# Kernel optimization log

Hardware: AMD Instinct MI355X
Metric: run time of the kernel (lower is better)

## Reference

```python
import jax, jax.numpy as jnp
import numpy as np

# Orbital structure for basis {A: [2s, 2p, 1d]} -> full_basis l values
LS = [0, 0, 1, 1, 2]
DIMS = [2 * l + 1 for l in LS]            # [1,1,3,3,5]
OFFS = np.concatenate([[0], np.cumsum(DIMS)]).astype(int)
NORB = int(sum(DIMS))                      # 13

# Upper-triangular orbital-pair layout of the flat feature vector
PAIRS = []
_off = 0
for _i in range(len(LS)):
    for _j in range(_i, len(LS)):
        PAIRS.append((_i, _j, _off))
        _off += DIMS[_i] * DIMS[_j]
FEAT_DIM = _off                            # 107

N_ATOMS, N_EDGES, N_KPTS = 256, 4096, 4


def _assemble_blocks(feat):
    """[B, FEAT_DIM] -> [B, NORB, NORB], upper-tri orbital blocks, 0.5 on diagonal pairs."""
    B = feat.shape[0]
    blk = jnp.zeros((B, NORB, NORB), feat.dtype)
    for (i, j, o) in PAIRS:
        di, dj = DIMS[i], DIMS[j]
        f = 0.5 if i == j else 1.0
        blk = blk.at[:, OFFS[i]:OFFS[i] + di, OFFS[j]:OFFS[j] + dj].set(
            f * feat[:, o:o + di * dj].reshape(B, di, dj))
    return blk


def setup_inputs() -> dict:
    key = jax.random.key(0)
    k1, k2, k3, k4, k5 = jax.random.split(key, 5)
    return {
        "orbpair_hopping": jax.random.normal(k1, (N_EDGES, FEAT_DIM), jnp.float32),
        "orbpair_onsite": jax.random.normal(k2, (N_ATOMS, FEAT_DIM), jnp.float32),
        "kpoints": jax.random.uniform(k3, (N_KPTS, 3), jnp.float32),
        "edge_cell_shift": jax.random.randint(k4, (N_EDGES, 3), -3, 4).astype(jnp.float32),
        "edge_index": jax.random.randint(k5, (2, N_EDGES), 0, N_ATOMS),
    }


def reference(orbpair_hopping, orbpair_onsite, kpoints, edge_cell_shift, edge_index):
    hop = _assemble_blocks(orbpair_hopping)      # [E, norb, norb]
    onsite = _assemble_blocks(orbpair_onsite)    # [N, norb, norb]
    N, K = onsite.shape[0], kpoints.shape[0]
    cplx = jnp.complex64

    # phase[k, e] = exp(-i 2pi k . R_e)
    phase = jnp.exp(-2j * jnp.pi * (kpoints @ edge_cell_shift.T)).astype(cplx)  # [K, E]

    # H(k) in block form [K, N, N, norb, norb]
    blk = jnp.zeros((K, N, N, NORB, NORB), cplx)
    ar = jnp.arange(N)
    blk = blk.at[:, ar, ar].set(onsite.astype(cplx)[None])  # diagonal onsite blocks
    ei, ej = edge_index[0], edge_index[1]
    blk = blk.at[:, ei, ej].add(phase[:, :, None, None] * hop.astype(cplx)[None])

    H = blk.transpose(0, 1, 3, 2, 4).reshape(K, N * NORB, N * NORB)
    return H + jnp.conj(jnp.swapaxes(H, 1, 2))  # hermitianize
```

## Files before the change

kernel.cpp:

```cpp
#include <hip/hip_runtime.h>

#define NORB 13
#define FEAT 107
#define TWO_PI 6.28318530717958647692f
#define NN 3328
#define NN2 (NN * NN)

__device__ __forceinline__ void map_pq(int p, int q, int& idx, float& scl) {
    const int DIMS[5] = {1, 1, 3, 3, 5};
    const int OFFS[5] = {0, 1, 2, 5, 8};
    idx = -1; scl = 0.0f;
    int o = 0;
    #pragma unroll
    for (int i = 0; i < 5; ++i) {
        #pragma unroll
        for (int j = i; j < 5; ++j) {
            int di = DIMS[i], dj = DIMS[j];
            if (p >= OFFS[i] && p < OFFS[i] + di && q >= OFFS[j] && q < OFFS[j] + dj) {
                idx = o + (p - OFFS[i]) * dj + (q - OFFS[j]);
                scl = (i == j) ? 0.5f : 1.0f;
            }
            o += di * dj;
        }
    }
}


__global__ void init_kernel(int4* __restrict__ head4, int* __restrict__ pairlist,
                            int* __restrict__ counter) {
    int t = blockIdx.x * blockDim.x + threadIdx.x;
    head4[t] = make_int4(-1, -1, -1, -1);
    if (t < 256) pairlist[t] = t * 257;
    if (t == 0) *counter = 256;
}

__global__ void fill_kernel(const int* __restrict__ eidx, const float* __restrict__ kpt,
                            const float* __restrict__ shf,
                            int* __restrict__ head, int* __restrict__ nxt,
                            int* __restrict__ pairlist, int* __restrict__ counter,
                            float* __restrict__ phases, int E, int K) {
    int tid = blockIdx.x * blockDim.x + threadIdx.x;
    if (tid >= 2 * E) return;
    int e = tid >> 1, dir = tid & 1;
    int ei = eidx[e], ej = eidx[E + e];
    int a = dir ? ej : ei;
    int b = dir ? ei : ej;
    int pid = a * 256 + b;
    int old = atomicExch(&head[pid], tid);
    nxt[tid] = old;
    if (old < 0 && a != b) {
        int pos = atomicAdd(counter, 1);
        pairlist[pos] = pid;
    }
    if (dir == 0) {
        float rx = shf[e * 3 + 0], ry = shf[e * 3 + 1], rz = shf[e * 3 + 2];
        for (int k = 0; k < K; ++k) {
            float th = -TWO_PI * (kpt[k * 3] * rx + kpt[k * 3 + 1] * ry + kpt[k * 3 + 2] * rz);
            float s, c;
            __sincosf(th, &s, &c);
            phases[(e * K + k) * 2]     = c;
            phases[(e * K + k) * 2 + 1] = s;
        }
    }
}

__global__ void zero_gated_kernel(float4* __restrict__ out4, const int* __restrict__ head,
                                  long n4) {
    long i = (long)blockIdx.x * blockDim.x + threadIdx.x;
    long stride = (long)gridDim.x * blockDim.x;
    float4 z = make_float4(0.f, 0.f, 0.f, 0.f);
    for (; i < n4; i += stride) {
        unsigned ci  = (unsigned)(i * 2);
        unsigned rem = ci % NN2;
        unsigned row = rem / NN;
        unsigned c   = rem - row * NN;
        unsigned a   = row / 13u;
        unsigned b0  = c / 13u;
        unsigned b1  = (c + 1u) / 13u;
        bool p0 = (a == b0) || head[a * 256u + b0] >= 0;
        bool p1 = (b1 == b0) ? p0 : ((a == b1) || head[a * 256u + b1] >= 0);
        if (!(p0 && p1)) out4[i] = z;
    }
}

__global__ void paint_kernel(const float* __restrict__ hop, const float* __restrict__ ons,
                             const int* __restrict__ head, const int* __restrict__ nxt,
                             const int* __restrict__ pairlist, const int* __restrict__ counter,
                             const float* __restrict__ phases, float* __restrict__ out,
                             int K) {
    int w = blockIdx.x;
    if (w >= *counter) return;
    int t = threadIdx.x;
    if (t >= NORB * NORB) return;
    int pid = pairlist[w];
    int a = pid >> 8, b = pid & 255;
    int p = t / NORB, q = t - p * NORB;
    int i0, i1; float s0, s1;
    map_pq(p, q, i0, s0);
    map_pq(q, p, i1, s1);
    float ar[4] = {0.f, 0.f, 0.f, 0.f}, ai[4] = {0.f, 0.f, 0.f, 0.f};
    if (a == b) {
        const float* f = ons + (long)a * FEAT;
        float v = 0.f;
        if (i0 >= 0) v += s0 * f[i0];
        if (i1 >= 0) v += s1 * f[i1];
        #pragma unroll
        for (int k = 0; k < 4; ++k) ar[k] += v;
    }
    for (int it = head[pid]; it >= 0; it = nxt[it]) {
        int e = it >> 1, dir = it & 1;
        float hv;
        if (dir == 0) hv = (i0 >= 0) ? s0 * hop[(long)e * FEAT + i0] : 0.f;
        else          hv = (i1 >= 0) ? s1 * hop[(long)e * FEAT + i1] : 0.f;
        const float* ph = phases + (long)e * K * 2;
        if (dir == 0) {
            #pragma unroll
            for (int k = 0; k < 4; ++k) { ar[k] += ph[2 * k] * hv; ai[k] += ph[2 * k + 1] * hv; }
        } else {
            #pragma unroll
            for (int k = 0; k < 4; ++k) { ar[k] += ph[2 * k] * hv; ai[k] -= ph[2 * k + 1] * hv; }
        }
    }
    long row = (long)a * NORB + p;
    long col = (long)b * NORB + q;
    #pragma unroll
    for (int k = 0; k < 4; ++k) {
        long off = (((long)k * NN + row) * NN + col) * 2;
        out[off]     = ar[k];
        out[off + 1] = ai[k];
    }
}


__global__ void zero_kernel(float4* __restrict__ out, long n4) {
    long i = (long)blockIdx.x * blockDim.x + threadIdx.x;
    long stride = (long)gridDim.x * blockDim.x;
    float4 z = make_float4(0.f, 0.f, 0.f, 0.f);
    for (; i < n4; i += stride) out[i] = z;
}

template <int CPX>
__global__ void onsite_kernel(const float* __restrict__ onsite, float* __restrict__ out,
                              int K, long nn) {
    int a = blockIdx.x;
    int t = threadIdx.x;
    if (t >= NORB * NORB) return;
    int p = t / NORB, q = t % NORB;
    int i1, i2; float s1, s2;
    map_pq(p, q, i1, s1);
    map_pq(q, p, i2, s2);
    const float* f = onsite + (long)a * FEAT;
    float v = 0.0f;
    if (i1 >= 0) v += s1 * f[i1];
    if (i2 >= 0) v += s2 * f[i2];
    long row = (long)a * NORB + p;
    long col = (long)a * NORB + q;
    for (int k = 0; k < K; ++k) {
        long off = (((long)k * nn + row) * nn + col) * CPX;
        out[off] = v;
    }
}

template <int CPX>
__global__ void edge_kernel(const float* __restrict__ hop, const float* __restrict__ kpts,
                            const float* __restrict__ shift, const int* __restrict__ eidx,
                            float* __restrict__ out, int E, int K, long nn) {
    int e = blockIdx.x;
    int t = threadIdx.x;
    __shared__ float phc[16], phs[16];
    int ei = eidx[e];
    int ej = eidx[E + e];
    if (t < K && t < 16) {
        float rx = shift[(long)e * 3 + 0];
        float ry = shift[(long)e * 3 + 1];
        float rz = shift[(long)e * 3 + 2];
        float th = -TWO_PI * (kpts[t * 3 + 0] * rx + kpts[t * 3 + 1] * ry + kpts[t * 3 + 2] * rz);
        float s, c;
        __sincosf(th, &s, &c);
        phc[t] = c; phs[t] = s;
    }
    __syncthreads();
    if (t >= NORB * NORB) return;
    int p = t / NORB, q = t % NORB;
    int idx; float scl;
    map_pq(p, q, idx, scl);
    if (idx < 0) return;
    float v = scl * hop[(long)e * FEAT + idx];
    long r1 = (long)ei * NORB + p, c1 = (long)ej * NORB + q;
    long r2 = (long)ej * NORB + q, c2 = (long)ei * NORB + p;
    for (int k = 0; k < K; ++k) {
        float pr = phc[k], pi = phs[k];
        long o1 = (((long)k * nn + r1) * nn + c1) * CPX;
        long o2 = (((long)k * nn + r2) * nn + c2) * CPX;
        atomicAdd(&out[o1], pr * v);
        atomicAdd(&out[o2], pr * v);
        if (CPX == 2) {
            atomicAdd(&out[o1 + 1], pi * v);
            atomicAdd(&out[o2 + 1], -pi * v);
        }
    }
}


extern "C" void kernel_launch(void* const* d_in, const int* in_sizes, int n_in,
                              void* d_out, int out_size, void* d_ws, size_t ws_size,
                              hipStream_t stream) {
    const float* hop  = (const float*)d_in[0];
    const float* ons  = (const float*)d_in[1];
    const float* kpt  = (const float*)d_in[2];
    const float* shf  = (const float*)d_in[3];
    const int*   eidx = (const int*)d_in[4];

    int E = in_sizes[0] / FEAT;
    int N = in_sizes[1] / FEAT;
    int K = in_sizes[2] / 3;
    long nn = (long)N * NORB;

    float* out = (float*)d_out;
    long knn2 = (long)K * nn * nn * 2;

    size_t off_head  = 0;
    size_t off_next  = off_head + 65536 * sizeof(int);
    size_t off_plist = off_next + (size_t)2 * E * sizeof(int);
    size_t off_cnt   = off_plist + (size_t)(256 + 2 * E) * sizeof(int);
    size_t off_phase = (off_cnt + 4 + 127) & ~(size_t)127;
    size_t ws_need   = off_phase + (size_t)E * K * 2 * sizeof(float);

    bool fast = (N == 256) && (K == 4) && (nn == NN) &&
                ((long)out_size == knn2) && (ws_size >= ws_need);

    if (fast) {
        char* ws = (char*)d_ws;
        int*   head   = (int*)(ws + off_head);
        int*   nxt    = (int*)(ws + off_next);
        int*   plist  = (int*)(ws + off_plist);
        int*   cnt    = (int*)(ws + off_cnt);
        float* phases = (float*)(ws + off_phase);

        init_kernel<<<64, 256, 0, stream>>>((int4*)head, plist, cnt);
        int fill_blocks = (2 * E + 255) / 256;
        fill_kernel<<<fill_blocks, 256, 0, stream>>>(eidx, kpt, shf, head, nxt,
                                                     plist, cnt, phases, E, K);
        long n4 = (long)out_size / 4;
        zero_gated_kernel<<<2048, 256, 0, stream>>>((float4*)out, head, n4);
        paint_kernel<<<256 + 2 * E, 192, 0, stream>>>(hop, ons, head, nxt, plist,
                                                      cnt, phases, out, K);
    } else {
        int cpx = ((long)out_size >= knn2) ? 2 : 1;
        long n4 = (long)out_size / 4;
        zero_kernel<<<2048, 256, 0, stream>>>((float4*)out, n4);
        if (cpx == 2) {
            onsite_kernel<2><<<N, 192, 0, stream>>>(ons, out, K, nn);
            edge_kernel<2><<<E, 192, 0, stream>>>(hop, kpt, shf, eidx, out, E, K, nn);
        } else {
            onsite_kernel<1><<<N, 192, 0, stream>>>(ons, out, K, nn);
            edge_kernel<1><<<E, 192, 0, stream>>>(hop, kpt, shf, eidx, out, E, K, nn);
        }
    }
}
```

Baseline: 80.97 us.

## Fuse gated zeroing and block painting into one kernel with per-row zero blocks

```diff
diff --git a/kernel.cpp b/kernel.cpp
--- a/kernel.cpp
+++ b/kernel.cpp
@@ -4,7 +4,7 @@
 #define FEAT 107
 #define TWO_PI 6.28318530717958647692f
 #define NN 3328
-#define NN2 (NN * NN)
+#define NROW 13312
 
 __device__ __forceinline__ void map_pq(int p, int q, int& idx, float& scl) {
     const int DIMS[5] = {1, 1, 3, 3, 5};
@@ -64,70 +64,75 @@
     }
 }
 
-__global__ void zero_gated_kernel(float4* __restrict__ out4, const int* __restrict__ head,
-                                  long n4) {
-    long i = (long)blockIdx.x * blockDim.x + threadIdx.x;
-    long stride = (long)gridDim.x * blockDim.x;
-    float4 z = make_float4(0.f, 0.f, 0.f, 0.f);
-    for (; i < n4; i += stride) {
-        unsigned ci  = (unsigned)(i * 2);
-        unsigned rem = ci % NN2;
-        unsigned row = rem / NN;
-        unsigned c   = rem - row * NN;
-        unsigned a   = row / 13u;
-        unsigned b0  = c / 13u;
-        unsigned b1  = (c + 1u) / 13u;
-        bool p0 = (a == b0) || head[a * 256u + b0] >= 0;
-        bool p1 = (b1 == b0) ? p0 : ((a == b1) || head[a * 256u + b1] >= 0);
-        if (!(p0 && p1)) out4[i] = z;
-    }
-}
-
-__global__ void paint_kernel(const float* __restrict__ hop, const float* __restrict__ ons,
-                             const int* __restrict__ head, const int* __restrict__ nxt,
-                             const int* __restrict__ pairlist, const int* __restrict__ counter,
-                             const float* __restrict__ phases, float* __restrict__ out,
-                             int K) {
-    int w = blockIdx.x;
-    if (w >= *counter) return;
+__global__ __launch_bounds__(256)
+void fused_kernel(const float* __restrict__ hop, const float* __restrict__ ons,
+                  const int* __restrict__ head, const int* __restrict__ nxt,
+                  const int* __restrict__ pairlist, const int* __restrict__ counter,
+                  const float* __restrict__ phases, float* __restrict__ out,
+                  int npaint) {
     int t = threadIdx.x;
-    if (t >= NORB * NORB) return;
-    int pid = pairlist[w];
-    int a = pid >> 8, b = pid & 255;
-    int p = t / NORB, q = t - p * NORB;
-    int i0, i1; float s0, s1;
-    map_pq(p, q, i0, s0);
-    map_pq(q, p, i1, s1);
-    float ar[4] = {0.f, 0.f, 0.f, 0.f}, ai[4] = {0.f, 0.f, 0.f, 0.f};
-    if (a == b) {
-        const float* f = ons + (long)a * FEAT;
-        float v = 0.f;
-        if (i0 >= 0) v += s0 * f[i0];
-        if (i1 >= 0) v += s1 * f[i1];
+    if ((int)blockIdx.x < npaint) {
+        int w = blockIdx.x;
+        if (w >= *counter) return;
+        if (t >= NORB * NORB) return;
+        int pid = pairlist[w];
+        int a = pid >> 8, b = pid & 255;
+        int p = t / NORB, q = t - p * NORB;
+        int i0, i1; float s0, s1;
+        map_pq(p, q, i0, s0);
+        map_pq(q, p, i1, s1);
+        float ar[4] = {0.f, 0.f, 0.f, 0.f}, ai[4] = {0.f, 0.f, 0.f, 0.f};
+        if (a == b) {
+            const float* f = ons + (long)a * FEAT;
+            float v = 0.f;
+            if (i0 >= 0) v += s0 * f[i0];
+            if (i1 >= 0) v += s1 * f[i1];
+            #pragma unroll
+            for (int k = 0; k < 4; ++k) ar[k] += v;
+        }
+        for (int it = head[pid]; it >= 0; it = nxt[it]) {
+            int e = it >> 1, dir = it & 1;
+            float hv;
+            if (dir == 0) hv = (i0 >= 0) ? s0 * hop[(long)e * FEAT + i0] : 0.f;
+            else          hv = (i1 >= 0) ? s1 * hop[(long)e * FEAT + i1] : 0.f;
+            const float* ph = phases + (long)e * 8;
+            if (dir == 0) {
+                #pragma unroll
+                for (int k = 0; k < 4; ++k) { ar[k] += ph[2*k] * hv; ai[k] += ph[2*k+1] * hv; }
+            } else {
+                #pragma unroll
+                for (int k = 0; k < 4; ++k) { ar[k] += ph[2*k] * hv; ai[k] -= ph[2*k+1] * hv; }
+            }
+        }
+        long row = (long)a * NORB + p;
+        long col = (long)b * NORB + q;
         #pragma unroll
-        for (int k = 0; k < 4; ++k) ar[k] += v;
-    }
-    for (int it = head[pid]; it >= 0; it = nxt[it]) {
-        int e = it >> 1, dir = it & 1;
-        float hv;
-        if (dir == 0) hv = (i0 >= 0) ? s0 * hop[(long)e * FEAT + i0] : 0.f;
-        else          hv = (i1 >= 0) ? s1 * hop[(long)e * FEAT + i1] : 0.f;
-        const float* ph = phases + (long)e * K * 2;
-        if (dir == 0) {
-            #pragma unroll
-            for (int k = 0; k < 4; ++k) { ar[k] += ph[2 * k] * hv; ai[k] += ph[2 * k + 1] * hv; }
-        } else {
-            #pragma unroll
-            for (int k = 0; k < 4; ++k) { ar[k] += ph[2 * k] * hv; ai[k] -= ph[2 * k + 1] * hv; }
-        }
-    }
-    long row = (long)a * NORB + p;
-    long col = (long)b * NORB + q;
-    #pragma unroll
-    for (int k = 0; k < 4; ++k) {
-        long off = (((long)k * NN + row) * NN + col) * 2;
-        out[off]     = ar[k];
-        out[off + 1] = ai[k];
+        for (int k = 0; k < 4; ++k) {
+            long off = (((long)k * NN + row) * NN + col) * 2;
+            out[off]     = ar[k];
+            out[off + 1] = ai[k];
+        }
+    } else {
+        int r = blockIdx.x - npaint;
+        unsigned rl = (unsigned)r % NN;
+        unsigned a  = rl / 13u;
+        __shared__ unsigned char pnt[256];
+        pnt[t] = (t == (int)a) ? 1 : (head[a * 256u + (unsigned)t] >= 0 ? 1 : 0);
+        __syncthreads();
+        long rowbase = (long)r * (NN * 2);
+        float4 z4 = make_float4(0.f, 0.f, 0.f, 0.f);
+        float2 z2 = make_float2(0.f, 0.f);
+        for (int f = t; f < NN / 2; f += 256) {
+            int c0 = 2 * f, c1 = 2 * f + 1;
+            int b0 = c0 / 13, b1 = c1 / 13;
+            bool p0 = pnt[b0] != 0;
+            bool p1 = (b1 == b0) ? p0 : (pnt[b1] != 0);
+            if (p0 && p1) continue;
+            long off = rowbase + 4l * f;
+            if (!p0 && !p1)      *(float4*)(out + off)     = z4;
+            else if (!p0)        *(float2*)(out + off)     = z2;
+            else                 *(float2*)(out + off + 2) = z2;
+        }
     }
 }
 
@@ -238,13 +243,11 @@
         float* phases = (float*)(ws + off_phase);
 
         init_kernel<<<64, 256, 0, stream>>>((int4*)head, plist, cnt);
-        int fill_blocks = (2 * E + 255) / 256;
-        fill_kernel<<<fill_blocks, 256, 0, stream>>>(eidx, kpt, shf, head, nxt,
-                                                     plist, cnt, phases, E, K);
-        long n4 = (long)out_size / 4;
-        zero_gated_kernel<<<2048, 256, 0, stream>>>((float4*)out, head, n4);
-        paint_kernel<<<256 + 2 * E, 192, 0, stream>>>(hop, ons, head, nxt, plist,
-                                                      cnt, phases, out, K);
+        fill_kernel<<<(2 * E + 255) / 256, 256, 0, stream>>>(eidx, kpt, shf, head, nxt,
+                                                             plist, cnt, phases, E, K);
+        int npaint = 256 + 2 * E;
+        fused_kernel<<<npaint + NROW, 256, 0, stream>>>(hop, ons, head, nxt, plist,
+                                                        cnt, phases, out, npaint);
     } else {
         int cpx = ((long)out_size >= knn2) ? 2 : 1;
         long n4 = (long)out_size / 4;
```

Result: no change. 80.24 us (-0.9%).
